# Kernel optimization log

Hardware: AMD Instinct MI355X
Metric: run time of the kernel (lower is better)

The kernel has to match this reference:

```python
import jax, jax.numpy as jnp
import numpy as np

N_NODES = 50000
N_EDGES = 800000
N_FEAT = 256
HIDDEN = 64
N_CLASSES = 16
T_END = 3.0  # opt['time']; rk4 takes one step over [0, 3]


def spline_conv(x, src, dst, p, W, R, b, n):
    """SplineConv, dim=1, kernel_size=2, degree=1 open B-spline, aggr='mean'.
    x: [n, Cin]; src/dst: [E]; p: [E,1] pseudo-coords in [0,1];
    W: [2, Cin, Cout]; R: [Cin, Cout]; b: [Cout]."""
    xj = x[src]  # gather source node features [E, Cin]
    # basis weights for K=2, degree=1: (1-p) on kernel 0, p on kernel 1
    msg = ((1.0 - p) * xj) @ W[0] + (p * xj) @ W[1]  # [E, Cout]
    agg = jax.ops.segment_sum(msg, dst, num_segments=n)
    deg = jax.ops.segment_sum(jnp.ones((msg.shape[0], 1), msg.dtype), dst, num_segments=n)
    return agg / jnp.maximum(deg, 1.0) + x @ R + b


def setup_inputs() -> dict:
    key = jax.random.key(0)
    ks = jax.random.split(key, 20)
    x = jax.random.normal(ks[0], (N_NODES, N_FEAT), jnp.float32)
    edge_attr = jax.random.uniform(ks[1], (N_EDGES, 1), jnp.float32)
    src = jax.random.randint(ks[2], (N_EDGES,), 0, N_NODES)
    dst = jax.random.randint(ks[3], (N_EDGES,), 0, N_NODES)

    def w(k, shape, fan_in):
        s = 1.0 / np.sqrt(fan_in)
        return jax.random.uniform(k, shape, jnp.float32, -s, s)

    # conv1: num_features -> hidden
    W1 = w(ks[4], (2, N_FEAT, HIDDEN), N_FEAT)
    R1 = w(ks[5], (N_FEAT, HIDDEN), N_FEAT)
    b1 = jnp.zeros((HIDDEN,), jnp.float32)
    # ODE func: two stacked SplineConvs hidden -> hidden
    Wa = w(ks[6], (2, HIDDEN, HIDDEN), HIDDEN)
    Ra = w(ks[7], (HIDDEN, HIDDEN), HIDDEN)
    ba = jnp.zeros((HIDDEN,), jnp.float32)
    Wb = w(ks[8], (2, HIDDEN, HIDDEN), HIDDEN)
    Rb = w(ks[9], (HIDDEN, HIDDEN), HIDDEN)
    bb = jnp.zeros((HIDDEN,), jnp.float32)
    # conv2: hidden -> num_classes
    W2 = w(ks[10], (2, HIDDEN, N_CLASSES), HIDDEN)
    R2 = w(ks[11], (HIDDEN, N_CLASSES), HIDDEN)
    b2 = jnp.zeros((N_CLASSES,), jnp.float32)

    return dict(x=x, edge_attr=edge_attr, src=src, dst=dst,
                W1=W1, R1=R1, b1=b1, Wa=Wa, Ra=Ra, ba=ba,
                Wb=Wb, Rb=Rb, bb=bb, W2=W2, R2=R2, b2=b2)


def reference(x, edge_attr, src, dst, W1, R1, b1, Wa, Ra, ba, Wb, Rb, bb, W2, R2, b2):
    n = x.shape[0]
    p = edge_attr
    h = jnp.tanh(spline_conv(x, src, dst, p, W1, R1, b1, n))
    # dropout is identity in eval mode

    def f(y):  # GCNLayer: two stacked SplineConvs, no activation
        y = spline_conv(y, src, dst, p, Wa, Ra, ba, n)
        return spline_conv(y, src, dst, p, Wb, Rb, bb, n)

    # single RK4 step from t=0 to t=T_END (torchdiffeq fixed-grid rk4 on s_span=[0,3])
    k1 = f(h)
    k2 = f(h + 0.5 * T_END * k1)
    k3 = f(h + 0.5 * T_END * k2)
    k4 = f(h + T_END * k3)
    h = h + (T_END / 6.0) * (k1 + 2.0 * k2 + 2.0 * k3 + k4)

    out = jnp.tanh(spline_conv(h, src, dst, p, W2, R2, b2, n))
    return jax.nn.log_softmax(out, axis=1)
```

## Files before the change

kernel.cpp:

```cpp
#include <hip/hip_runtime.h>
#include <math.h>

static inline int ceil_div(int a, int b) { return (a + b - 1) / b; }


__global__ __launch_bounds__(256) void hist_kernel(const int* __restrict__ dst,
                                                   int* __restrict__ deg, int E) {
    int e = blockIdx.x * 256 + threadIdx.x;
    if (e < E) atomicAdd(&deg[dst[e]], 1);
}

__global__ __launch_bounds__(1024) void scan_build(const int* __restrict__ deg,
                                                   int* __restrict__ rowp,
                                                   float* __restrict__ invd,
                                                   int n, int E) {
    __shared__ int sums[1024];
    int t = threadIdx.x;
    int chunk = (n + 1023) >> 10;
    int start = t * chunk;
    int end = start + chunk; if (end > n) end = n;
    int s = 0;
    for (int i = start; i < end; ++i) s += deg[i];
    sums[t] = s;
    __syncthreads();
    for (int off = 1; off < 1024; off <<= 1) {
        int add = (t >= off) ? sums[t - off] : 0;
        __syncthreads();
        sums[t] += add;
        __syncthreads();
    }
    int run = sums[t] - s;
    for (int i = start; i < end; ++i) {
        rowp[i] = run;
        int d = deg[i];
        run += d;
        invd[i] = 1.0f / (float)(d > 1 ? d : 1);
    }
    if (t == 0) rowp[n] = E;
}

__global__ __launch_bounds__(256) void scatter_kernel(const int* __restrict__ src,
                                                      const int* __restrict__ dst,
                                                      const float* __restrict__ p,
                                                      const int* __restrict__ rowp,
                                                      int* __restrict__ fill,
                                                      int* __restrict__ es,
                                                      float* __restrict__ ep, int E) {
    int e = blockIdx.x * 256 + threadIdx.x;
    if (e >= E) return;
    int d = dst[e];
    int pos = rowp[d] + atomicAdd(&fill[d], 1);
    es[pos] = src[e];
    ep[pos] = p[e];
}

__global__ __launch_bounds__(256) void pack_cat3(const float* __restrict__ W,
                                                 const float* __restrict__ R,
                                                 float* __restrict__ out, int K, int C) {
    int idx = blockIdx.x * 256 + threadIdx.x;
    int M = 3 * C;
    if (idx >= K * M) return;
    int k = idx / M, c = idx % M;
    float v;
    if (c < C)            v = W[k * C + c];
    else if (c < 2 * C)   v = W[K * C + k * C + (c - C)];
    else                  v = R[k * C + (c - 2 * C)];
    out[idx] = v;
}


__global__ __launch_bounds__(256) void edge_agg64(const float* __restrict__ x,
                                                  const int* __restrict__ rowp,
                                                  const int* __restrict__ es,
                                                  const float* __restrict__ ep,
                                                  const float* __restrict__ invd,
                                                  float* __restrict__ agg, int n) {
    int gid = blockIdx.x * 256 + threadIdx.x;
    int node = gid >> 6;
    if (node >= n) return;
    int c = gid & 63;
    int e = rowp[node], eend = rowp[node + 1];
    float asum = 0.f, ap = 0.f;
    for (; e + 4 <= eend; e += 4) {
        int s0 = es[e], s1 = es[e + 1], s2 = es[e + 2], s3 = es[e + 3];
        float p0 = ep[e], p1 = ep[e + 1], p2 = ep[e + 2], p3 = ep[e + 3];
        float v0 = x[(size_t)s0 * 64 + c];
        float v1 = x[(size_t)s1 * 64 + c];
        float v2 = x[(size_t)s2 * 64 + c];
        float v3 = x[(size_t)s3 * 64 + c];
        asum += (v0 + v1) + (v2 + v3);
        ap = fmaf(p0, v0, fmaf(p1, v1, fmaf(p2, v2, fmaf(p3, v3, ap))));
    }
    for (; e < eend; ++e) {
        int s = es[e]; float pe = ep[e];
        float v = x[(size_t)s * 64 + c];
        asum += v; ap = fmaf(pe, v, ap);
    }
    float w = invd[node];
    agg[(size_t)node * 128 + c]      = (asum - ap) * w;
    agg[(size_t)node * 128 + 64 + c] = ap * w;
}

__global__ __launch_bounds__(256) void edge_tf64(const float* __restrict__ yz,
                                                 const int* __restrict__ rowp,
                                                 const int* __restrict__ es,
                                                 const float* __restrict__ ep,
                                                 const float* __restrict__ invd,
                                                 const float* __restrict__ base,
                                                 float* __restrict__ out, int n) {
    int gid = blockIdx.x * 256 + threadIdx.x;
    int node = gid >> 6;
    if (node >= n) return;
    int c = gid & 63;
    int e = rowp[node], eend = rowp[node + 1];
    float a = 0.f;
    for (; e + 4 <= eend; e += 4) {
        int s0 = es[e], s1 = es[e + 1], s2 = es[e + 2], s3 = es[e + 3];
        float p0 = ep[e], p1 = ep[e + 1], p2 = ep[e + 2], p3 = ep[e + 3];
        float y0 = yz[(size_t)s0 * 128 + c],      z0 = yz[(size_t)s0 * 128 + 64 + c];
        float y1 = yz[(size_t)s1 * 128 + c],      z1 = yz[(size_t)s1 * 128 + 64 + c];
        float y2 = yz[(size_t)s2 * 128 + c],      z2 = yz[(size_t)s2 * 128 + 64 + c];
        float y3 = yz[(size_t)s3 * 128 + c],      z3 = yz[(size_t)s3 * 128 + 64 + c];
        a += fmaf(p0, z0 - y0, y0);
        a += fmaf(p1, z1 - y1, y1);
        a += fmaf(p2, z2 - y2, y2);
        a += fmaf(p3, z3 - y3, y3);
    }
    for (; e < eend; ++e) {
        int s = es[e]; float pe = ep[e];
        float y = yz[(size_t)s * 128 + c], z = yz[(size_t)s * 128 + 64 + c];
        a += fmaf(pe, z - y, y);
    }
    size_t idx = (size_t)node * 64 + c;
    out[idx] = tanhf(a * invd[node] + base[idx]);
}

__global__ __launch_bounds__(256) void edge_tf16_lsm(const float* __restrict__ yz,
                                                     const int* __restrict__ rowp,
                                                     const int* __restrict__ es,
                                                     const float* __restrict__ ep,
                                                     const float* __restrict__ invd,
                                                     const float* __restrict__ base,
                                                     float* __restrict__ out, int n) {
    int gid = blockIdx.x * 256 + threadIdx.x;
    int node = gid >> 4;
    if (node >= n) return;
    int c = gid & 15;
    int e = rowp[node], eend = rowp[node + 1];
    float a = 0.f;
    for (; e + 4 <= eend; e += 4) {
        int s0 = es[e], s1 = es[e + 1], s2 = es[e + 2], s3 = es[e + 3];
        float p0 = ep[e], p1 = ep[e + 1], p2 = ep[e + 2], p3 = ep[e + 3];
        float y0 = yz[(size_t)s0 * 32 + c],      z0 = yz[(size_t)s0 * 32 + 16 + c];
        float y1 = yz[(size_t)s1 * 32 + c],      z1 = yz[(size_t)s1 * 32 + 16 + c];
        float y2 = yz[(size_t)s2 * 32 + c],      z2 = yz[(size_t)s2 * 32 + 16 + c];
        float y3 = yz[(size_t)s3 * 32 + c],      z3 = yz[(size_t)s3 * 32 + 16 + c];
        a += fmaf(p0, z0 - y0, y0);
        a += fmaf(p1, z1 - y1, y1);
        a += fmaf(p2, z2 - y2, y2);
        a += fmaf(p3, z3 - y3, y3);
    }
    for (; e < eend; ++e) {
        int s = es[e]; float pe = ep[e];
        float y = yz[(size_t)s * 32 + c], z = yz[(size_t)s * 32 + 16 + c];
        a += fmaf(pe, z - y, y);
    }
    float o = tanhf(a * invd[node] + base[(size_t)node * 16 + c]);
    float m = o;
    #pragma unroll
    for (int off = 8; off >= 1; off >>= 1) m = fmaxf(m, __shfl_xor(m, off, 16));
    float ex = expf(o - m);
    float s = ex;
    #pragma unroll
    for (int off = 8; off >= 1; off >>= 1) s += __shfl_xor(s, off, 16);
    out[(size_t)node * 16 + c] = (o - m) - logf(s);
}

__global__ __launch_bounds__(256) void gemm_tiled(
    const float* __restrict__ A0, int lda0, int K0,
    const float* __restrict__ A1, int lda1,
    const float* __restrict__ B,
    int n, int K, int M,
    float* __restrict__ out0, int w0, const float* __restrict__ bias0,
    float* __restrict__ out1, int w1, const float* __restrict__ bias1,
    int split, int mode,
    const float* __restrict__ hbuf, const float* __restrict__ acc_in,
    float* __restrict__ acc_out, float* __restrict__ t_out,
    float c1, float c2, float c3) {
    __shared__ __align__(16) float As[16][68];
    __shared__ __align__(16) float Bs[16][68];
    const int t = threadIdx.x;
    const int row0 = blockIdx.x * 64;
    const int col0 = blockIdx.y * 64;
    const int ty = t >> 4, tx = t & 15;
    const int lrow = t >> 2, lk = (t & 3) << 2;
    const int bkk = t >> 4, bcol = (t & 15) << 2;
    float acc[4][4];
    #pragma unroll
    for (int i = 0; i < 4; ++i)
        #pragma unroll
        for (int j = 0; j < 4; ++j) acc[i][j] = 0.f;

    for (int k0 = 0; k0 < K; k0 += 16) {
        float4 av = make_float4(0.f, 0.f, 0.f, 0.f);
        {
            int r = row0 + lrow;
            if (r < n) {
                int kk = k0 + lk;
                const float* src = (kk < K0)
                    ? (A0 + (size_t)r * lda0 + kk)
                    : (A1 + (size_t)r * lda1 + (kk - K0));
                av = *reinterpret_cast<const float4*>(src);
            }
        }
        float4 bv = make_float4(0.f, 0.f, 0.f, 0.f);
        {
            int c = col0 + bcol;
            int kk = k0 + bkk;
            if (c < M) bv = *reinterpret_cast<const float4*>(B + (size_t)kk * M + c);
        }
        As[lk + 0][lrow] = av.x; As[lk + 1][lrow] = av.y;
        As[lk + 2][lrow] = av.z; As[lk + 3][lrow] = av.w;
        *reinterpret_cast<float4*>(&Bs[bkk][bcol]) = bv;
        __syncthreads();
        #pragma unroll
        for (int kk = 0; kk < 16; ++kk) {
            float4 a4 = *reinterpret_cast<const float4*>(&As[kk][ty << 2]);
            float4 b4 = *reinterpret_cast<const float4*>(&Bs[kk][tx << 2]);
            float aa[4] = {a4.x, a4.y, a4.z, a4.w};
            float bb[4] = {b4.x, b4.y, b4.z, b4.w};
            #pragma unroll
            for (int i = 0; i < 4; ++i)
                #pragma unroll
                for (int j = 0; j < 4; ++j)
                    acc[i][j] = fmaf(aa[i], bb[j], acc[i][j]);
        }
        __syncthreads();
    }

    #pragma unroll
    for (int i = 0; i < 4; ++i) {
        int r = row0 + (ty << 2) + i;
        if (r >= n) continue;
        #pragma unroll
        for (int j = 0; j < 4; ++j) {
            int c = col0 + (tx << 2) + j;
            if (c >= M) continue;
            float v = acc[i][j];
            if (mode == 0) {
                if (c < split) {
                    if (bias0) v += bias0[c];
                    out0[(size_t)r * w0 + c] = v;
                } else {
                    int cc = c - split;
                    if (bias1) v += bias1[cc];
                    out1[(size_t)r * w1 + cc] = v;
                }
            } else {
                if (bias0) v += bias0[c];
                size_t idx = (size_t)r * 64 + c;
                float an = (acc_in ? acc_in[idx] : 0.f) + c3 * v;
                acc_out[idx] = an;
                t_out[idx] = hbuf[idx] + c1 * v + c2 * an;
            }
        }
    }
}


static void hidden_conv(hipStream_t stream, const float* in, float* big0,
                        const int* rowp, const int* es, const float* ep,
                        const float* invd, const float* Bc, const float* bias, int n,
                        int mode, float* out_plain,
                        const float* h, const float* acc_in, float* acc_out,
                        float* t_out, float c1, float c2, float c3) {
    edge_agg64<<<ceil_div(n * 64, 256), 256, 0, stream>>>(in, rowp, es, ep, invd, big0, n);
    dim3 g(ceil_div(n, 64), 1);
    gemm_tiled<<<g, 256, 0, stream>>>(big0, 128, 128, in, 64, Bc, n, 192, 64,
                                      out_plain, 64, bias, nullptr, 0, nullptr, 64, mode,
                                      h, acc_in, acc_out, t_out, c1, c2, c3);
}

extern "C" void kernel_launch(void* const* d_in, const int* in_sizes, int n_in,
                              void* d_out, int out_size, void* d_ws, size_t ws_size,
                              hipStream_t stream) {
    const float* x  = (const float*)d_in[0];
    const float* pE = (const float*)d_in[1];
    const int*   sr = (const int*)d_in[2];
    const int*   ds = (const int*)d_in[3];
    const float* W1 = (const float*)d_in[4];
    const float* R1 = (const float*)d_in[5];
    const float* b1 = (const float*)d_in[6];
    const float* Wa = (const float*)d_in[7];
    const float* Ra = (const float*)d_in[8];
    const float* ba = (const float*)d_in[9];
    const float* Wb = (const float*)d_in[10];
    const float* Rb = (const float*)d_in[11];
    const float* bb = (const float*)d_in[12];
    const float* W2 = (const float*)d_in[13];
    const float* R2 = (const float*)d_in[14];
    const float* b2 = (const float*)d_in[15];
    const int n = in_sizes[0] / 256;
    const int E = in_sizes[2];
    float* out = (float*)d_out;

    char* w = (char*)d_ws;
    auto alloc = [&](size_t bytes) -> void* {
        void* ptr = (void*)w;
        w += (bytes + 255) & ~(size_t)255;
        return ptr;
    };
    int*   deg  = (int*)alloc((size_t)n * 4);
    int*   fill = (int*)alloc((size_t)n * 4);
    int*   rowp = (int*)alloc((size_t)(n + 1) * 4);
    float* invd = (float*)alloc((size_t)n * 4);
    int*   es   = (int*)alloc((size_t)E * 4);
    float* ep   = (float*)alloc((size_t)E * 4);
    float* Bc1  = (float*)alloc((size_t)256 * 192 * 4);
    float* Bca  = (float*)alloc((size_t)192 * 64 * 4);
    float* Bcb  = (float*)alloc((size_t)192 * 64 * 4);
    float* Bc2  = (float*)alloc((size_t)64 * 48 * 4);
    float* big0 = (float*)alloc((size_t)n * 128 * 4);
    float* big1 = (float*)alloc((size_t)n * 64 * 4);
    float* h    = (float*)alloc((size_t)n * 64 * 4);
    float* u    = (float*)alloc((size_t)n * 64 * 4);
    float* tb   = (float*)alloc((size_t)n * 64 * 4);
    float* acc  = (float*)alloc((size_t)n * 64 * 4);

    hipMemsetAsync(deg, 0, (size_t)n * 4, stream);
    hipMemsetAsync(fill, 0, (size_t)n * 4, stream);

    pack_cat3<<<ceil_div(256 * 192, 256), 256, 0, stream>>>(W1, R1, Bc1, 256, 64);
    pack_cat3<<<ceil_div(64 * 48, 256), 256, 0, stream>>>(W2, R2, Bc2, 64, 16);
    hipMemcpyAsync(Bca, Wa, (size_t)8192 * 4, hipMemcpyDeviceToDevice, stream);
    hipMemcpyAsync(Bca + 8192, Ra, (size_t)4096 * 4, hipMemcpyDeviceToDevice, stream);
    hipMemcpyAsync(Bcb, Wb, (size_t)8192 * 4, hipMemcpyDeviceToDevice, stream);
    hipMemcpyAsync(Bcb + 8192, Rb, (size_t)4096 * 4, hipMemcpyDeviceToDevice, stream);

    hist_kernel<<<ceil_div(E, 256), 256, 0, stream>>>(ds, deg, E);
    scan_build<<<1, 1024, 0, stream>>>(deg, rowp, invd, n, E);
    scatter_kernel<<<ceil_div(E, 256), 256, 0, stream>>>(sr, ds, pE, rowp, fill, es, ep, E);

    {
        dim3 g(ceil_div(n, 64), 3);
        gemm_tiled<<<g, 256, 0, stream>>>(x, 256, 256, nullptr, 0, Bc1, n, 256, 192,
                                          big0, 128, nullptr, big1, 64, b1, 128, 0,
                                          nullptr, nullptr, nullptr, nullptr, 0.f, 0.f, 0.f);
        edge_tf64<<<ceil_div(n * 64, 256), 256, 0, stream>>>(big0, rowp, es, ep, invd,
                                                             big1, h, n);
    }

    hidden_conv(stream, h, big0, rowp, es, ep, invd, Bca, ba, n, 0, u,
                nullptr, nullptr, nullptr, nullptr, 0.f, 0.f, 0.f);
    hidden_conv(stream, u, big0, rowp, es, ep, invd, Bcb, bb, n, 1, nullptr,
                h, nullptr, acc, tb, 1.5f, 0.f, 1.f);
    hidden_conv(stream, tb, big0, rowp, es, ep, invd, Bca, ba, n, 0, u,
                nullptr, nullptr, nullptr, nullptr, 0.f, 0.f, 0.f);
    hidden_conv(stream, u, big0, rowp, es, ep, invd, Bcb, bb, n, 1, nullptr,
                h, acc, acc, tb, 1.5f, 0.f, 2.f);
    hidden_conv(stream, tb, big0, rowp, es, ep, invd, Bca, ba, n, 0, u,
                nullptr, nullptr, nullptr, nullptr, 0.f, 0.f, 0.f);
    hidden_conv(stream, u, big0, rowp, es, ep, invd, Bcb, bb, n, 1, nullptr,
                h, acc, acc, tb, 3.f, 0.f, 2.f);
    hidden_conv(stream, tb, big0, rowp, es, ep, invd, Bca, ba, n, 0, u,
                nullptr, nullptr, nullptr, nullptr, 0.f, 0.f, 0.f);
    hidden_conv(stream, u, big0, rowp, es, ep, invd, Bcb, bb, n, 1, nullptr,
                h, acc, acc, tb, 0.f, 0.5f, 1.f);

    {
        dim3 g(ceil_div(n, 64), 1);
        gemm_tiled<<<g, 256, 0, stream>>>(tb, 64, 64, nullptr, 0, Bc2, n, 64, 48,
                                          big0, 32, nullptr, big1, 16, b2, 32, 0,
                                          nullptr, nullptr, nullptr, nullptr, 0.f, 0.f, 0.f);
        edge_tf16_lsm<<<ceil_div(n * 16, 256), 256, 0, stream>>>(big0, rowp, es, ep, invd,
                                                                 big1, out, n);
    }
}
```

Measured before the change: 1.064 ms.

## Parallelize CSR scan, sort edges per node, vectorize edge aggregation with float4

Replaces the single-block 1024-thread prefix scan with a three-pass multi-block scan. Edge placement now scatters edge ids, then each node insertion-sorts its own edge list and fills es/ep, so the CSR order is deterministic and follows source order. The edge aggregation kernels now use 16 threads per node with float4 gathers instead of 64 scalar loads per node, which cuts instruction count and widens memory transactions. The cost is fewer threads in flight and two extra small kernels during CSR construction.

New measurement: 951.7 us. 10.6% less time.

```diff
diff --git a/kernel.cpp b/kernel.cpp
--- a/kernel.cpp
+++ b/kernel.cpp
@@ -10,48 +10,112 @@
     if (e < E) atomicAdd(&deg[dst[e]], 1);
 }
 
-__global__ __launch_bounds__(1024) void scan_build(const int* __restrict__ deg,
-                                                   int* __restrict__ rowp,
-                                                   float* __restrict__ invd,
-                                                   int n, int E) {
-    __shared__ int sums[1024];
+__global__ __launch_bounds__(256) void scan_blocksum(const int* __restrict__ deg,
+                                                     int* __restrict__ bsum, int n) {
+    __shared__ int red[256];
     int t = threadIdx.x;
-    int chunk = (n + 1023) >> 10;
-    int start = t * chunk;
-    int end = start + chunk; if (end > n) end = n;
+    int base = blockIdx.x * 2048 + t * 8;
     int s = 0;
-    for (int i = start; i < end; ++i) s += deg[i];
-    sums[t] = s;
+    #pragma unroll
+    for (int i = 0; i < 8; ++i) {
+        int idx = base + i;
+        if (idx < n) s += deg[idx];
+    }
+    red[t] = s;
     __syncthreads();
-    for (int off = 1; off < 1024; off <<= 1) {
-        int add = (t >= off) ? sums[t - off] : 0;
-        __syncthreads();
-        sums[t] += add;
-        __syncthreads();
-    }
-    int run = sums[t] - s;
-    for (int i = start; i < end; ++i) {
-        rowp[i] = run;
-        int d = deg[i];
-        run += d;
-        invd[i] = 1.0f / (float)(d > 1 ? d : 1);
-    }
-    if (t == 0) rowp[n] = E;
-}
-
-__global__ __launch_bounds__(256) void scatter_kernel(const int* __restrict__ src,
-                                                      const int* __restrict__ dst,
-                                                      const float* __restrict__ p,
-                                                      const int* __restrict__ rowp,
-                                                      int* __restrict__ fill,
-                                                      int* __restrict__ es,
-                                                      float* __restrict__ ep, int E) {
+    #pragma unroll
+    for (int off = 128; off >= 1; off >>= 1) {
+        if (t < off) red[t] += red[t + off];
+        __syncthreads();
+    }
+    if (t == 0) bsum[blockIdx.x] = red[0];
+}
+
+__global__ __launch_bounds__(256) void scan_tops(int* __restrict__ bsum, int nb) {
+    __shared__ int sh[256];
+    int t = threadIdx.x;
+    int orig = (t < nb) ? bsum[t] : 0;
+    sh[t] = orig;
+    __syncthreads();
+    for (int off = 1; off < 256; off <<= 1) {
+        int add = (t >= off) ? sh[t - off] : 0;
+        __syncthreads();
+        sh[t] += add;
+        __syncthreads();
+    }
+    if (t < nb) bsum[t] = sh[t] - orig;
+}
+
+__global__ __launch_bounds__(256) void scan_final(const int* __restrict__ deg,
+                                                  const int* __restrict__ bsum,
+                                                  int* __restrict__ rowp,
+                                                  float* __restrict__ invd,
+                                                  int n, int E) {
+    __shared__ int sh[256];
+    int t = threadIdx.x;
+    int base = blockIdx.x * 2048 + t * 8;
+    int loc[8];
+    int s = 0;
+    #pragma unroll
+    for (int i = 0; i < 8; ++i) {
+        int idx = base + i;
+        int d = (idx < n) ? deg[idx] : 0;
+        loc[i] = d;
+        s += d;
+    }
+    sh[t] = s;
+    __syncthreads();
+    for (int off = 1; off < 256; off <<= 1) {
+        int add = (t >= off) ? sh[t - off] : 0;
+        __syncthreads();
+        sh[t] += add;
+        __syncthreads();
+    }
+    int run = bsum[blockIdx.x] + (sh[t] - s);
+    #pragma unroll
+    for (int i = 0; i < 8; ++i) {
+        int idx = base + i;
+        if (idx < n) {
+            rowp[idx] = run;
+            int d = loc[i];
+            run += d;
+            invd[idx] = 1.0f / (float)(d > 1 ? d : 1);
+        }
+    }
+    if (blockIdx.x == 0 && t == 0) rowp[n] = E;
+}
+
+__global__ __launch_bounds__(256) void scatter_idx(const int* __restrict__ dst,
+                                                   const int* __restrict__ rowp,
+                                                   int* __restrict__ fill,
+                                                   int* __restrict__ ei, int E) {
     int e = blockIdx.x * 256 + threadIdx.x;
     if (e >= E) return;
     int d = dst[e];
     int pos = rowp[d] + atomicAdd(&fill[d], 1);
-    es[pos] = src[e];
-    ep[pos] = p[e];
+    ei[pos] = e;
+}
+
+__global__ __launch_bounds__(256) void sort_fill(const int* __restrict__ rowp,
+                                                 int* __restrict__ ei,
+                                                 const int* __restrict__ src,
+                                                 const float* __restrict__ p,
+                                                 int* __restrict__ es,
+                                                 float* __restrict__ ep, int n) {
+    int node = blockIdx.x * 256 + threadIdx.x;
+    if (node >= n) return;
+    int b = rowp[node], e = rowp[node + 1];
+    for (int i = b + 1; i < e; ++i) {
+        int key = ei[i];
+        int j = i - 1;
+        while (j >= b && ei[j] > key) { ei[j + 1] = ei[j]; --j; }
+        ei[j + 1] = key;
+    }
+    for (int i = b; i < e; ++i) {
+        int id = ei[i];
+        es[i] = src[id];
+        ep[i] = p[id];
+    }
 }
 
 __global__ __launch_bounds__(256) void pack_cat3(const float* __restrict__ W,
@@ -69,70 +133,91 @@
 }
 
 
-__global__ __launch_bounds__(256) void edge_agg64(const float* __restrict__ x,
-                                                  const int* __restrict__ rowp,
-                                                  const int* __restrict__ es,
-                                                  const float* __restrict__ ep,
-                                                  const float* __restrict__ invd,
-                                                  float* __restrict__ agg, int n) {
+__global__ __launch_bounds__(256) void edge_agg64_v4(const float* __restrict__ x,
+                                                     const int* __restrict__ rowp,
+                                                     const int* __restrict__ es,
+                                                     const float* __restrict__ ep,
+                                                     const float* __restrict__ invd,
+                                                     float* __restrict__ agg, int n) {
     int gid = blockIdx.x * 256 + threadIdx.x;
-    int node = gid >> 6;
+    int node = gid >> 4;
     if (node >= n) return;
-    int c = gid & 63;
+    int c4 = (gid & 15) << 2;
     int e = rowp[node], eend = rowp[node + 1];
-    float asum = 0.f, ap = 0.f;
+    float sx = 0.f, sy = 0.f, sz = 0.f, sw = 0.f;
+    float px = 0.f, py = 0.f, pz = 0.f, pw = 0.f;
     for (; e + 4 <= eend; e += 4) {
         int s0 = es[e], s1 = es[e + 1], s2 = es[e + 2], s3 = es[e + 3];
         float p0 = ep[e], p1 = ep[e + 1], p2 = ep[e + 2], p3 = ep[e + 3];
-        float v0 = x[(size_t)s0 * 64 + c];
-        float v1 = x[(size_t)s1 * 64 + c];
-        float v2 = x[(size_t)s2 * 64 + c];
-        float v3 = x[(size_t)s3 * 64 + c];
-        asum += (v0 + v1) + (v2 + v3);
-        ap = fmaf(p0, v0, fmaf(p1, v1, fmaf(p2, v2, fmaf(p3, v3, ap))));
+        float4 v0 = *reinterpret_cast<const float4*>(&x[(size_t)s0 * 64 + c4]);
+        float4 v1 = *reinterpret_cast<const float4*>(&x[(size_t)s1 * 64 + c4]);
+        float4 v2 = *reinterpret_cast<const float4*>(&x[(size_t)s2 * 64 + c4]);
+        float4 v3 = *reinterpret_cast<const float4*>(&x[(size_t)s3 * 64 + c4]);
+        sx += (v0.x + v1.x) + (v2.x + v3.x);
+        sy += (v0.y + v1.y) + (v2.y + v3.y);
+        sz += (v0.z + v1.z) + (v2.z + v3.z);
+        sw += (v0.w + v1.w) + (v2.w + v3.w);
+        px = fmaf(p0, v0.x, fmaf(p1, v1.x, fmaf(p2, v2.x, fmaf(p3, v3.x, px))));
+        py = fmaf(p0, v0.y, fmaf(p1, v1.y, fmaf(p2, v2.y, fmaf(p3, v3.y, py))));
+        pz = fmaf(p0, v0.z, fmaf(p1, v1.z, fmaf(p2, v2.z, fmaf(p3, v3.z, pz))));
+        pw = fmaf(p0, v0.w, fmaf(p1, v1.w, fmaf(p2, v2.w, fmaf(p3, v3.w, pw))));
     }
     for (; e < eend; ++e) {
-        int s = es[e]; float pe = ep[e];
-        float v = x[(size_t)s * 64 + c];
-        asum += v; ap = fmaf(pe, v, ap);
+        int s = es[e];
+        float pe = ep[e];
+        float4 v = *reinterpret_cast<const float4*>(&x[(size_t)s * 64 + c4]);
+        sx += v.x; sy += v.y; sz += v.z; sw += v.w;
+        px = fmaf(pe, v.x, px); py = fmaf(pe, v.y, py);
+        pz = fmaf(pe, v.z, pz); pw = fmaf(pe, v.w, pw);
     }
     float w = invd[node];
-    agg[(size_t)node * 128 + c]      = (asum - ap) * w;
-    agg[(size_t)node * 128 + 64 + c] = ap * w;
-}
-
-__global__ __launch_bounds__(256) void edge_tf64(const float* __restrict__ yz,
-                                                 const int* __restrict__ rowp,
-                                                 const int* __restrict__ es,
-                                                 const float* __restrict__ ep,
-                                                 const float* __restrict__ invd,
-                                                 const float* __restrict__ base,
-                                                 float* __restrict__ out, int n) {
+    float4 a0 = make_float4((sx - px) * w, (sy - py) * w, (sz - pz) * w, (sw - pw) * w);
+    float4 a1 = make_float4(px * w, py * w, pz * w, pw * w);
+    *reinterpret_cast<float4*>(&agg[(size_t)node * 128 + c4]) = a0;
+    *reinterpret_cast<float4*>(&agg[(size_t)node * 128 + 64 + c4]) = a1;
+}
+
+__global__ __launch_bounds__(256) void edge_tf64_v4(const float* __restrict__ yz,
+                                                    const int* __restrict__ rowp,
+                                                    const int* __restrict__ es,
+                                                    const float* __restrict__ ep,
+                                                    const float* __restrict__ invd,
+                                                    const float* __restrict__ base,
+                                                    float* __restrict__ out, int n) {
     int gid = blockIdx.x * 256 + threadIdx.x;
-    int node = gid >> 6;
+    int node = gid >> 4;
     if (node >= n) return;
-    int c = gid & 63;
+    int c4 = (gid & 15) << 2;
     int e = rowp[node], eend = rowp[node + 1];
-    float a = 0.f;
-    for (; e + 4 <= eend; e += 4) {
-        int s0 = es[e], s1 = es[e + 1], s2 = es[e + 2], s3 = es[e + 3];
-        float p0 = ep[e], p1 = ep[e + 1], p2 = ep[e + 2], p3 = ep[e + 3];
-        float y0 = yz[(size_t)s0 * 128 + c],      z0 = yz[(size_t)s0 * 128 + 64 + c];
-        float y1 = yz[(size_t)s1 * 128 + c],      z1 = yz[(size_t)s1 * 128 + 64 + c];
-        float y2 = yz[(size_t)s2 * 128 + c],      z2 = yz[(size_t)s2 * 128 + 64 + c];
-        float y3 = yz[(size_t)s3 * 128 + c],      z3 = yz[(size_t)s3 * 128 + 64 + c];
-        a += fmaf(p0, z0 - y0, y0);
-        a += fmaf(p1, z1 - y1, y1);
-        a += fmaf(p2, z2 - y2, y2);
-        a += fmaf(p3, z3 - y3, y3);
+    float ax = 0.f, ay = 0.f, az = 0.f, aw = 0.f;
+    for (; e + 2 <= eend; e += 2) {
+        int s0 = es[e], s1 = es[e + 1];
+        float p0 = ep[e], p1 = ep[e + 1];
+        float4 y0 = *reinterpret_cast<const float4*>(&yz[(size_t)s0 * 128 + c4]);
+        float4 z0 = *reinterpret_cast<const float4*>(&yz[(size_t)s0 * 128 + 64 + c4]);
+        float4 y1 = *reinterpret_cast<const float4*>(&yz[(size_t)s1 * 128 + c4]);
+        float4 z1 = *reinterpret_cast<const float4*>(&yz[(size_t)s1 * 128 + 64 + c4]);
+        ax += fmaf(p0, z0.x - y0.x, y0.x) + fmaf(p1, z1.x - y1.x, y1.x);
+        ay += fmaf(p0, z0.y - y0.y, y0.y) + fmaf(p1, z1.y - y1.y, y1.y);
+        az += fmaf(p0, z0.z - y0.z, y0.z) + fmaf(p1, z1.z - y1.z, y1.z);
+        aw += fmaf(p0, z0.w - y0.w, y0.w) + fmaf(p1, z1.w - y1.w, y1.w);
     }
     for (; e < eend; ++e) {
-        int s = es[e]; float pe = ep[e];
-        float y = yz[(size_t)s * 128 + c], z = yz[(size_t)s * 128 + 64 + c];
-        a += fmaf(pe, z - y, y);
-    }
-    size_t idx = (size_t)node * 64 + c;
-    out[idx] = tanhf(a * invd[node] + base[idx]);
+        int s = es[e];
+        float pe = ep[e];
+        float4 y = *reinterpret_cast<const float4*>(&yz[(size_t)s * 128 + c4]);
+        float4 z = *reinterpret_cast<const float4*>(&yz[(size_t)s * 128 + 64 + c4]);
+        ax += fmaf(pe, z.x - y.x, y.x);
+        ay += fmaf(pe, z.y - y.y, y.y);
+        az += fmaf(pe, z.z - y.z, y.z);
+        aw += fmaf(pe, z.w - y.w, y.w);
+    }
+    float w = invd[node];
+    size_t idx = (size_t)node * 64 + c4;
+    float4 b = *reinterpret_cast<const float4*>(&base[idx]);
+    float4 o = make_float4(tanhf(fmaf(ax, w, b.x)), tanhf(fmaf(ay, w, b.y)),
+                           tanhf(fmaf(az, w, b.z)), tanhf(fmaf(aw, w, b.w)));
+    *reinterpret_cast<float4*>(&out[idx]) = o;
 }
 
 __global__ __launch_bounds__(256) void edge_tf16_lsm(const float* __restrict__ yz,
@@ -274,7 +359,7 @@
                         int mode, float* out_plain,
                         const float* h, const float* acc_in, float* acc_out,
                         float* t_out, float c1, float c2, float c3) {
-    edge_agg64<<<ceil_div(n * 64, 256), 256, 0, stream>>>(in, rowp, es, ep, invd, big0, n);
+    edge_agg64_v4<<<ceil_div(n * 16, 256), 256, 0, stream>>>(in, rowp, es, ep, invd, big0, n);
     dim3 g(ceil_div(n, 64), 1);
     gemm_tiled<<<g, 256, 0, stream>>>(big0, 128, 128, in, 64, Bc, n, 192, 64,
                                       out_plain, 64, bias, nullptr, 0, nullptr, 64, mode,
@@ -310,10 +395,13 @@
         w += (bytes + 255) & ~(size_t)255;
         return ptr;
     };
+    int nscan = ceil_div(n, 2048);
     int*   deg  = (int*)alloc((size_t)n * 4);
     int*   fill = (int*)alloc((size_t)n * 4);
     int*   rowp = (int*)alloc((size_t)(n + 1) * 4);
     float* invd = (float*)alloc((size_t)n * 4);
+    int*   bsum = (int*)alloc((size_t)256 * 4);
+    int*   ei   = (int*)alloc((size_t)E * 4);
     int*   es   = (int*)alloc((size_t)E * 4);
     float* ep   = (float*)alloc((size_t)E * 4);
     float* Bc1  = (float*)alloc((size_t)256 * 192 * 4);
@@ -338,16 +426,19 @@
     hipMemcpyAsync(Bcb + 8192, Rb, (size_t)4096 * 4, hipMemcpyDeviceToDevice, stream);
 
     hist_kernel<<<ceil_div(E, 256), 256, 0, stream>>>(ds, deg, E);
-    scan_build<<<1, 1024, 0, stream>>>(deg, rowp, invd, n, E);
-    scatter_kernel<<<ceil_div(E, 256), 256, 0, stream>>>(sr, ds, pE, rowp, fill, es, ep, E);
+    scan_blocksum<<<nscan, 256, 0, stream>>>(deg, bsum, n);
+    scan_tops<<<1, 256, 0, stream>>>(bsum, nscan);
+    scan_final<<<nscan, 256, 0, stream>>>(deg, bsum, rowp, invd, n, E);
+    scatter_idx<<<ceil_div(E, 256), 256, 0, stream>>>(ds, rowp, fill, ei, E);
+    sort_fill<<<ceil_div(n, 256), 256, 0, stream>>>(rowp, ei, sr, pE, es, ep, n);
 
     {
         dim3 g(ceil_div(n, 64), 3);
         gemm_tiled<<<g, 256, 0, stream>>>(x, 256, 256, nullptr, 0, Bc1, n, 256, 192,
                                           big0, 128, nullptr, big1, 64, b1, 128, 0,
                                           nullptr, nullptr, nullptr, nullptr, 0.f, 0.f, 0.f);
-        edge_tf64<<<ceil_div(n * 64, 256), 256, 0, stream>>>(big0, rowp, es, ep, invd,
-                                                             big1, h, n);
+        edge_tf64_v4<<<ceil_div(n * 16, 256), 256, 0, stream>>>(big0, rowp, es, ep, invd,
+                                                                big1, h, n);
     }
 
     hidden_conv(stream, h, big0, rowp, es, ep, invd, Bca, ba, n, 0, u,
```
